# Kernel tuning notes

Measured on AMD Instinct MI355X. Metric: run time of the kernel, lower is better.

## Reference

```python
import jax, jax.numpy as jnp
import numpy as np

B, T, U, V, H, KA, KO = 64, 600, 64, 80, 512, 10, 20


def setup_inputs() -> dict:
    key = jax.random.key(0)
    ks = jax.random.split(key, 12)
    std = 0.075
    p = lambda k, shape: jax.random.normal(k, shape, jnp.float32) * std
    return dict(
        char_seq=jax.random.randint(ks[0], (B, U), 0, V),
        char_mask=jnp.ones((B, U), jnp.float32),
        strokes=jax.random.normal(ks[1], (B, T, 3), jnp.float32),
        strokes_mask=jnp.ones((B, T), jnp.float32),
        lstm0_Wih=p(ks[2], (4 * H, 3 + V)), lstm0_Whh=p(ks[3], (4 * H, H)), lstm0_b=jnp.zeros((4 * H,), jnp.float32),
        win_W=p(ks[4], (3 * KA, H)), win_b=jnp.zeros((3 * KA,), jnp.float32),
        lstm1_Wih=p(ks[5], (4 * H, 3 + V + H)), lstm1_Whh=p(ks[6], (4 * H, H)), lstm1_b=jnp.zeros((4 * H,), jnp.float32),
        lstm2_Wih=p(ks[7], (4 * H, 3 + V + H)), lstm2_Whh=p(ks[8], (4 * H, H)), lstm2_b=jnp.zeros((4 * H,), jnp.float32),
        fc_W=p(ks[9], (6 * KO + 1, 3 * H)), fc_b=jnp.zeros((6 * KO + 1,), jnp.float32),
    )


def _lstm_cell(gates_x, h, c, Whh):
    # gates_x already contains x@Wih.T + b; PyTorch gate order: i, f, g, o
    gates = gates_x + h @ Whh.T
    i, f, g, o = jnp.split(gates, 4, axis=-1)
    c = jax.nn.sigmoid(f) * c + jax.nn.sigmoid(i) * jnp.tanh(g)
    h = jax.nn.sigmoid(o) * jnp.tanh(c)
    return h, c


def _run_lstm(x, Wih, Whh, b):
    # x: [B, T, F]; precompute input projection once (big GEMM), scan only on h.
    gx = jnp.einsum('btf,gf->btg', x, Wih) + b  # [B,T,4H]
    h0 = jnp.zeros((x.shape[0], H), x.dtype)
    c0 = jnp.zeros((x.shape[0], H), x.dtype)

    def step(carry, g_t):
        h, c = carry
        h, c = _lstm_cell(g_t, h, c, Whh)
        return (h, c), h

    _, hs = jax.lax.scan(step, (h0, c0), gx.transpose(1, 0, 2))
    return hs.transpose(1, 0, 2)  # [B,T,H]


def _forward(char_seq, char_mask, strokes,
             lstm0_Wih, lstm0_Whh, lstm0_b, win_W, win_b,
             lstm1_Wih, lstm1_Whh, lstm1_b, lstm2_Wih, lstm2_Whh, lstm2_b,
             fc_W, fc_b):
    char_oh = jax.nn.one_hot(char_seq, V, dtype=jnp.float32) * char_mask[..., None]  # [B,U,V]
    u_grid = jnp.arange(U, dtype=jnp.float32)  # char positions

    h0 = jnp.zeros((B, H), jnp.float32)
    c0 = jnp.zeros((B, H), jnp.float32)
    w0 = jnp.zeros((B, V), jnp.float32)
    k0 = jnp.zeros((B, KA), jnp.float32)

    def step(carry, x_t):
        h, c, w, k = carry
        inp = jnp.concatenate([x_t, w], axis=-1)  # [B, 3+V]
        gates = inp @ lstm0_Wih.T + lstm0_b
        h, c = _lstm_cell(gates, h, c, lstm0_Whh)
        # Gaussian attention window (Graves 2013)
        p = h @ win_W.T + win_b  # [B, 3K]
        alpha, beta, kap_hat = jnp.split(jnp.exp(p), 3, axis=-1)
        k = k + kap_hat  # [B,K]
        phi = jnp.sum(alpha[:, :, None] * jnp.exp(-beta[:, :, None] * (k[:, :, None] - u_grid) ** 2), axis=1)
        phi = phi * char_mask  # [B,U]
        w = jnp.einsum('bu,buv->bv', phi, char_oh)
        return (h, c, w, k), (h, w)

    _, (h_seq, w_seq) = jax.lax.scan(step, (h0, c0, w0, k0), strokes.transpose(1, 0, 2))
    lstm0_out = h_seq.transpose(1, 0, 2)   # [B,T,H]
    attn_out = w_seq.transpose(1, 0, 2)    # [B,T,V]

    lstm1_out = _run_lstm(jnp.concatenate([strokes, attn_out, lstm0_out], -1), lstm1_Wih, lstm1_Whh, lstm1_b)
    lstm2_out = _run_lstm(jnp.concatenate([strokes, attn_out, lstm1_out], -1), lstm2_Wih, lstm2_Whh, lstm2_b)

    final = jnp.einsum('bth,gh->btg', jnp.concatenate([lstm0_out, lstm1_out, lstm2_out], -1), fc_W) + fc_b
    # parse_outputs: split [2K, 2K, K, K, 1]
    myu = final[..., : 2 * KO]
    log_sigma = final[..., 2 * KO: 4 * KO]
    pi = final[..., 4 * KO: 5 * KO]
    rho = final[..., 5 * KO: 6 * KO]
    eos = final[..., 6 * KO:]
    log_pi = jax.nn.log_softmax(pi, axis=-1)
    rho = jnp.tanh(rho)
    eos = jax.nn.sigmoid(-eos)
    myu = myu.reshape(myu.shape[:-1] + (KO, 2))
    log_sigma = log_sigma.reshape(log_sigma.shape[:-1] + (KO, 2))
    return (log_pi, myu, log_sigma, rho, eos)


def reference(char_seq, char_mask, strokes, strokes_mask,
              lstm0_Wih, lstm0_Whh, lstm0_b, win_W, win_b,
              lstm1_Wih, lstm1_Whh, lstm1_b, lstm2_Wih, lstm2_Whh, lstm2_b,
              fc_W, fc_b):
    # strokes_mask is unused by forward() in the original module (only in losses)
    return _forward(char_seq, char_mask, strokes,
                    lstm0_Wih, lstm0_Whh, lstm0_b, win_W, win_b,
                    lstm1_Wih, lstm1_Whh, lstm1_b, lstm2_Wih, lstm2_Whh, lstm2_b,
                    fc_W, fc_b)
```

## Files before the change

kernel.cpp:

```cpp
#include <hip/hip_runtime.h>
#include <math.h>

#define B_ 64
#define T_ 600
#define U_ 64
#define V_ 80
#define H_ 512
#define KA_ 10
#define KO_ 20

#define S0_ 600
#define S12_ 1108

__device__ __forceinline__ float sigmf(float x){ return 1.0f/(1.0f+expf(-x)); }

__device__ __forceinline__ int coh_load_i32(const int* p){
    int v;
    asm volatile("global_load_dword %0, %1, off sc0 sc1\n\ts_waitcnt vmcnt(0)"
                 : "=v"(v) : "v"(p) : "memory");
    return v;
}
__device__ __forceinline__ void coh_store_f32(float* p, float v){
    asm volatile("global_store_dword %0, %1, off sc0 sc1" :: "v"(p), "v"(v) : "memory");
}
__device__ __forceinline__ void coh_store_u32(unsigned* p, unsigned v){
    asm volatile("global_store_dword %0, %1, off sc0 sc1" :: "v"(p), "v"(v) : "memory");
}
__device__ __forceinline__ void spin_ge(int* p, int target){
    while (coh_load_i32(p) < target) __builtin_amdgcn_s_sleep(4);
}
#define BLOCK_WAIT(p, tgt) do { if (threadIdx.x == 0) spin_ge((p), (tgt)); __syncthreads(); } while (0)

__device__ __forceinline__ float blo(unsigned u){ return __uint_as_float(u << 16); }
__device__ __forceinline__ float bhi(unsigned u){ return __uint_as_float(u & 0xffff0000u); }
__device__ __forceinline__ unsigned pack_bf16(float a, float b){
    return ((__float_as_uint(a) + 0x8000u) >> 16) | ((__float_as_uint(b) + 0x8000u) & 0xffff0000u);
}

__global__ __launch_bounds__(64) void k_prep(
    const float* __restrict__ W0ih, const float* __restrict__ W0hh,
    const float* __restrict__ W1ih, const float* __restrict__ W1hh,
    const float* __restrict__ W2ih, const float* __restrict__ W2hh,
    float* __restrict__ wpad)
{
    int r = blockIdx.x;
    int tid = threadIdx.x;
    if (r < 2048){
        float* dst = wpad + (size_t)r*S0_;
        const float* sih = W0ih + (size_t)r*83;
        const float* shh = W0hh + (size_t)r*512;
        if (tid < 3) dst[tid] = sih[tid];
        if (tid == 3) dst[3] = 0.f;
        for (int v=tid; v<V_; v+=64) dst[4+v] = sih[3+v];
        for (int k=tid; k<H_; k+=64) dst[84+k] = shh[k];
    } else {
        int rr = r - 2048;
        int layer = rr >> 11;
        int row = rr & 2047;
        const float* sih = (layer==0 ? W1ih : W2ih) + (size_t)row*595;
        const float* shh = (layer==0 ? W1hh : W2hh) + (size_t)row*512;
        float* dst = wpad + (size_t)2048*S0_ + ((size_t)layer*2048 + row)*S12_;
        if (tid < 3) dst[tid] = sih[tid];
        if (tid == 3) dst[3] = 0.f;
        for (int v=tid; v<V_; v+=64) dst[4+v] = sih[3+v];
        for (int k=tid; k<H_; k+=64) dst[84+k] = sih[83+k];
        for (int k=tid; k<H_; k+=64) dst[596+k] = shh[k];
    }
}

__global__ __launch_bounds__(256, 2) void k_pipe(
    const float* __restrict__ strokes,
    const int*   __restrict__ char_seq,
    const float* __restrict__ char_mask,
    const float* __restrict__ wpad,
    const float* __restrict__ winW, const float* __restrict__ winb,
    const float* __restrict__ b0, const float* __restrict__ b1, const float* __restrict__ b2,
    float* __restrict__ out0, float* __restrict__ out1, float* __restrict__ out2,
    unsigned* __restrict__ attnb, int* __restrict__ sync)
{
    __builtin_amdgcn_fence(__ATOMIC_ACQUIRE, "agent");

    int* c0 = sync;
    int* c1 = sync + 640;
    int* c2 = sync + 1280;
    int* cw = sync + 1920;

    const int bid = blockIdx.x;
    const int tid = threadIdx.x;
    const int b   = tid & 63;
    const int g   = tid >> 6;

    __shared__ float part[4][4][64];
    __shared__ float pp[30][8];
    __shared__ float sa[KA_], sbv[KA_], sk[KA_], skst[KA_];
    __shared__ float sphi[U_];
    __shared__ float satt[V_];
    __shared__ int   sseq[U_];
    __shared__ float smask[U_];

    if (bid >= 384){
        const int wb = bid - 384;
        if (tid < U_){ sseq[tid] = char_seq[wb*U_+tid]; smask[tid] = char_mask[wb*U_+tid]; }
        __syncthreads();
        for (int t=0; t<T_; ++t){
            BLOCK_WAIT(&c0[t], 128);
            if (tid < 240){
                int r = tid >> 3, p8 = tid & 7;
                const float4* hp = (const float4*)(out0 + (size_t)t*32768);
                const float4* wr = (const float4*)(winW + (size_t)r*H_);
                float acc = 0.f;
                int kq0 = p8*16;
                #pragma unroll 4
                for (int i=0; i<16; ++i){
                    float4 xv = hp[(size_t)(kq0+i)*64 + wb];
                    float4 wv = wr[kq0+i];
                    acc += xv.x*wv.x + xv.y*wv.y + xv.z*wv.z + xv.w*wv.w;
                }
                pp[r][p8] = acc;
            }
            __syncthreads();
            if (tid < 30){
                float p = winb[tid];
                #pragma unroll
                for (int i=0; i<8; ++i) p += pp[tid][i];
                float e = expf(p);
                if (tid < KA_) sa[tid] = e;
                else if (tid < 2*KA_) sbv[tid-KA_] = e;
                else {
                    int a2 = tid - 2*KA_;
                    float kn = ((t == 0) ? 0.f : skst[a2]) + e;
                    skst[a2] = kn; sk[a2] = kn;
                }
            }
            __syncthreads();
            if (tid < U_){
                float acc = 0.f;
                #pragma unroll
                for (int a=0; a<KA_; ++a){
                    float d = sk[a] - (float)tid;
                    acc += sa[a]*expf(-sbv[a]*d*d);
                }
                sphi[tid] = acc * smask[tid]*smask[tid];
            }
            __syncthreads();
            if (tid < V_){
                float wv = 0.f;
                for (int u=0; u<U_; ++u) wv += (sseq[u] == tid) ? sphi[u] : 0.f;
                satt[tid] = wv;
            }
            __syncthreads();
            if (tid < 40){
                unsigned pk = pack_bf16(satt[2*tid], satt[2*tid+1]);
                coh_store_u32(attnb + (size_t)t*2560 + (size_t)wb*40 + tid, pk);
            }
            __syncthreads();
            if (tid == 0) atomicAdd(&cw[t], 1);
        }
        return;
    }

    const int l  = bid >> 7;
    const int ub = (bid & 127) * 4;

    const float* wbase; const float* bias_p; const float* xprev; float* outp;
    int* cself; int* cprev; size_t wstride; int roff;
    if (l == 0){ wbase = wpad;                                          wstride = S0_;  bias_p = b0; outp = out0; xprev = nullptr; cself = c0; cprev = nullptr; roff = 84; }
    else if (l == 1){ wbase = wpad + (size_t)2048*S0_;                  wstride = S12_; bias_p = b1; outp = out1; xprev = out0;   cself = c1; cprev = c0;     roff = 596; }
    else { wbase = wpad + (size_t)2048*S0_ + (size_t)2048*S12_;         wstride = S12_; bias_p = b2; outp = out2; xprev = out1;   cself = c2; cprev = c1;     roff = 596; }

    const float* wr = wbase + ((size_t)g*H_ + ub)*wstride;
    const float* wr1 = wr + wstride;
    const float* wr2 = wr + 2*wstride;
    const float* wr3 = wr + 3*wstride;

    const int cu = ub + g;
    const float bgi = bias_p[0*H_+cu];
    const float bgf = bias_p[1*H_+cu];
    const float bgg = bias_p[2*H_+cu];
    const float bgo = bias_p[3*H_+cu];
    float creg = 0.f;

    for (int t=0; t<T_; ++t){
        float a0, a1, a2, a3;
        {
            const float* sr = strokes + ((size_t)b*T_ + t)*3;
            float sx=sr[0], sy=sr[1], sz=sr[2];
            a0 = sx*wr[0]  + sy*wr[1]  + sz*wr[2];
            a1 = sx*wr1[0] + sy*wr1[1] + sz*wr1[2];
            a2 = sx*wr2[0] + sy*wr2[1] + sz*wr2[2];
            a3 = sx*wr3[0] + sy*wr3[1] + sz*wr3[2];
        }
        if (t > 0){
            BLOCK_WAIT(&cself[t-1], 128);
            const float4* hp = (const float4*)(outp + (size_t)(t-1)*32768) + b;
            #pragma unroll 4
            for (int kq=0; kq<128; ++kq){
                float4 xv = hp[kq*64];
                float4 q0 = *(const float4*)(wr  + roff + kq*4);
                float4 q1 = *(const float4*)(wr1 + roff + kq*4);
                float4 q2 = *(const float4*)(wr2 + roff + kq*4);
                float4 q3 = *(const float4*)(wr3 + roff + kq*4);
                a0 += xv.x*q0.x + xv.y*q0.y + xv.z*q0.z + xv.w*q0.w;
                a1 += xv.x*q1.x + xv.y*q1.y + xv.z*q1.z + xv.w*q1.w;
                a2 += xv.x*q2.x + xv.y*q2.y + xv.z*q2.z + xv.w*q2.w;
                a3 += xv.x*q3.x + xv.y*q3.y + xv.z*q3.z + xv.w*q3.w;
            }
        }
        if (l > 0){
            BLOCK_WAIT(&cprev[t], 128);
            const float4* hp = (const float4*)(xprev + (size_t)t*32768) + b;
            #pragma unroll 4
            for (int kq=0; kq<128; ++kq){
                float4 xv = hp[kq*64];
                float4 q0 = *(const float4*)(wr  + 84 + kq*4);
                float4 q1 = *(const float4*)(wr1 + 84 + kq*4);
                float4 q2 = *(const float4*)(wr2 + 84 + kq*4);
                float4 q3 = *(const float4*)(wr3 + 84 + kq*4);
                a0 += xv.x*q0.x + xv.y*q0.y + xv.z*q0.z + xv.w*q0.w;
                a1 += xv.x*q1.x + xv.y*q1.y + xv.z*q1.z + xv.w*q1.w;
                a2 += xv.x*q2.x + xv.y*q2.y + xv.z*q2.z + xv.w*q2.w;
                a3 += xv.x*q3.x + xv.y*q3.y + xv.z*q3.z + xv.w*q3.w;
            }
        }
        {
            int ta = (l == 0) ? (t-1) : t;
            if (ta >= 0){
                BLOCK_WAIT(&cw[ta], 64);
                const uint4* ap = (const uint4*)(attnb + (size_t)ta*2560 + (size_t)b*40);
                #pragma unroll
                for (int j=0; j<10; ++j){
                    uint4 q = ap[j];
                    float x0 = blo(q.x), x1 = bhi(q.x), x2 = blo(q.y), x3 = bhi(q.y);
                    float x4 = blo(q.z), x5 = bhi(q.z), x6 = blo(q.w), x7 = bhi(q.w);
                    float4 qa, qb;
                    qa = *(const float4*)(wr  + 4 + 8*j); qb = *(const float4*)(wr  + 8 + 8*j);
                    a0 += x0*qa.x + x1*qa.y + x2*qa.z + x3*qa.w + x4*qb.x + x5*qb.y + x6*qb.z + x7*qb.w;
                    qa = *(const float4*)(wr1 + 4 + 8*j); qb = *(const float4*)(wr1 + 8 + 8*j);
                    a1 += x0*qa.x + x1*qa.y + x2*qa.z + x3*qa.w + x4*qb.x + x5*qb.y + x6*qb.z + x7*qb.w;
                    qa = *(const float4*)(wr2 + 4 + 8*j); qb = *(const float4*)(wr2 + 8 + 8*j);
                    a2 += x0*qa.x + x1*qa.y + x2*qa.z + x3*qa.w + x4*qb.x + x5*qb.y + x6*qb.z + x7*qb.w;
                    qa = *(const float4*)(wr3 + 4 + 8*j); qb = *(const float4*)(wr3 + 8 + 8*j);
                    a3 += x0*qa.x + x1*qa.y + x2*qa.z + x3*qa.w + x4*qb.x + x5*qb.y + x6*qb.z + x7*qb.w;
                }
            }
        }
        part[g][0][b] = a0;
        part[g][1][b] = a1;
        part[g][2][b] = a2;
        part[g][3][b] = a3;
        __syncthreads();
        {
            float gi  = part[0][g][b] + bgi;
            float gf  = part[1][g][b] + bgf;
            float gg_ = part[2][g][b] + bgg;
            float go  = part[3][g][b] + bgo;
            float cold = (t == 0) ? 0.f : creg;
            float cnew = sigmf(gf)*cold + sigmf(gi)*tanhf(gg_);
            creg = cnew;
            float h = sigmf(go)*tanhf(cnew);
            coh_store_f32(outp + (size_t)t*32768 + (size_t)(cu>>2)*256 + b*4 + (cu&3), h);
        }
        __syncthreads();
        if (tid == 0) atomicAdd(&cself[t], 1);
    }
}

__global__ __launch_bounds__(256) void k_fc(
    const float* __restrict__ out0, const float* __restrict__ out1, const float* __restrict__ out2,
    const float* __restrict__ fcW, const float* __restrict__ fcb, float* __restrict__ out)
{
    int t = blockIdx.x; int tid = threadIdx.x;
    int b = tid & 63; int gq = tid >> 6;
    __shared__ float smraw[128*65];

    float acc[31];
    #pragma unroll
    for (int i=0; i<31; ++i) acc[i] = 0.f;

    const float* outs[3] = {out0, out1, out2};
    for (int seg=0; seg<3; ++seg){
        const float* o = outs[seg] + (size_t)t*32768;
        for (int kc=0; kc<H_; kc+=128){
            __syncthreads();
            #pragma unroll
            for (int r=0; r<8; ++r){
                int idx = tid + 256*r;
                int kql = idx >> 6;
                int bb  = idx & 63;
                float4 v = *(const float4*)(o + (size_t)((kc>>2) + kql)*256 + bb*4);
                smraw[(4*kql+0)*65+bb] = v.x;
                smraw[(4*kql+1)*65+bb] = v.y;
                smraw[(4*kql+2)*65+bb] = v.z;
                smraw[(4*kql+3)*65+bb] = v.w;
            }
            __syncthreads();
            for (int kk=0; kk<128; kk+=4){
                float a0 = smraw[(kk+0)*65+b];
                float a1 = smraw[(kk+1)*65+b];
                float a2 = smraw[(kk+2)*65+b];
                float a3 = smraw[(kk+3)*65+b];
                int K = seg*H_ + kc + kk;
                #pragma unroll
                for (int i=0; i<30; ++i){
                    float4 w = *(const float4*)(fcW + (size_t)(gq+4*i)*1536 + K);
                    acc[i] += a0*w.x + a1*w.y + a2*w.z + a3*w.w;
                }
                if (gq == 0){
                    float4 w = *(const float4*)(fcW + (size_t)120*1536 + K);
                    acc[30] += a0*w.x + a1*w.y + a2*w.z + a3*w.w;
                }
            }
        }
    }
    __syncthreads();
    #pragma unroll
    for (int i=0; i<30; ++i) smraw[(gq+4*i)*64 + b] = acc[i] + fcb[gq+4*i];
    if (gq == 0) smraw[120*64 + b] = acc[30] + fcb[120];
    __syncthreads();

    if (tid < 64){
        size_t bt = (size_t)b*T_ + t;
        float* myu = out + 768000;
        #pragma unroll
        for (int q=0; q<10; ++q){
            float4 v;
            v.x = smraw[(4*q+0)*64+b]; v.y = smraw[(4*q+1)*64+b];
            v.z = smraw[(4*q+2)*64+b]; v.w = smraw[(4*q+3)*64+b];
            *(float4*)(myu + bt*40 + 4*q) = v;
        }
        float* lsg = out + 2304000;
        #pragma unroll
        for (int q=0; q<10; ++q){
            float4 v;
            v.x = smraw[(40+4*q+0)*64+b]; v.y = smraw[(40+4*q+1)*64+b];
            v.z = smraw[(40+4*q+2)*64+b]; v.w = smraw[(40+4*q+3)*64+b];
            *(float4*)(lsg + bt*40 + 4*q) = v;
        }
        float pi[KO_];
        float m = -1e30f;
        #pragma unroll
        for (int ko=0; ko<KO_; ++ko){ pi[ko] = smraw[(80+ko)*64+b]; m = fmaxf(m, pi[ko]); }
        float s = 0.f;
        #pragma unroll
        for (int ko=0; ko<KO_; ++ko) s += expf(pi[ko]-m);
        float lse = m + logf(s);
        #pragma unroll
        for (int q=0; q<5; ++q){
            float4 v;
            v.x = pi[4*q+0]-lse; v.y = pi[4*q+1]-lse; v.z = pi[4*q+2]-lse; v.w = pi[4*q+3]-lse;
            *(float4*)(out + bt*20 + 4*q) = v;
        }
        float* rho = out + 3840000;
        #pragma unroll
        for (int q=0; q<5; ++q){
            float4 v;
            v.x = tanhf(smraw[(100+4*q+0)*64+b]); v.y = tanhf(smraw[(100+4*q+1)*64+b]);
            v.z = tanhf(smraw[(100+4*q+2)*64+b]); v.w = tanhf(smraw[(100+4*q+3)*64+b]);
            *(float4*)(rho + bt*20 + 4*q) = v;
        }
        out[4608000 + bt] = 1.f/(1.f + expf(smraw[120*64+b]));
    }
}

extern "C" void kernel_launch(void* const* d_in, const int* in_sizes, int n_in,
                              void* d_out, int out_size, void* d_ws, size_t ws_size,
                              hipStream_t stream)
{
    const int*   char_seq  = (const int*)  d_in[0];
    const float* char_mask = (const float*)d_in[1];
    const float* strokes   = (const float*)d_in[2];
    const float* W0ih = (const float*)d_in[4];
    const float* W0hh = (const float*)d_in[5];
    const float* b0   = (const float*)d_in[6];
    const float* winW = (const float*)d_in[7];
    const float* winb = (const float*)d_in[8];
    const float* W1ih = (const float*)d_in[9];
    const float* W1hh = (const float*)d_in[10];
    const float* b1   = (const float*)d_in[11];
    const float* W2ih = (const float*)d_in[12];
    const float* W2hh = (const float*)d_in[13];
    const float* b2   = (const float*)d_in[14];
    const float* fcW  = (const float*)d_in[15];
    const float* fcb  = (const float*)d_in[16];

    float* ws   = (float*)d_ws;
    float*    out0  = ws;
    float*    out1  = out0 + 19660800;
    float*    out2  = out1 + 19660800;
    unsigned* attnb = (unsigned*)(out2 + 19660800);
    float*    wpad  = (float*)(attnb + 1536000);
    int*      sync  = (int*)(wpad + 5767168);

    hipMemsetAsync(sync, 0, 2560*sizeof(int), stream);

    hipLaunchKernelGGL(k_prep, dim3(6144), dim3(64), 0, stream,
        W0ih, W0hh, W1ih, W1hh, W2ih, W2hh, wpad);

    hipLaunchKernelGGL(k_pipe, dim3(448), dim3(256), 0, stream,
        strokes, char_seq, char_mask, wpad, winW, winb, b0, b1, b2,
        out0, out1, out2, attnb, sync);

    hipLaunchKernelGGL(k_fc, dim3(600), dim3(256), 0, stream,
        out0, out1, out2, fcW, fcb, (float*)d_out);
}
```

Measured before the change: 53.08 ms.

## Restructure LSTM pipeline: bf16 hidden states, 8 units per block, fewer blocks

Hidden-state outputs of all three LSTM layers are now stored as packed bf16 instead of fp32, which halves inter-block traffic and the fc input reads. Each pipeline block now has 512 threads, and each thread computes all four gates for one unit over the full K range. This removes the shared-memory cross-gate reduction and halves the number of LSTM blocks (64 per layer). The window blocks stage the hidden state in shared memory and use 480 threads for the projection. Layers 1 and 2 wait on all dependencies at once, and the spin sleep is shorter. The change risks reduced precision and a longer serial dot product per thread.

```diff
diff --git a/kernel.cpp b/kernel.cpp
--- a/kernel.cpp
+++ b/kernel.cpp
@@ -11,6 +11,10 @@
 
 #define S0_ 600
 #define S12_ 1108
+#define NLB_ 64
+#define NWB_ 64
+
+typedef unsigned u32x4 __attribute__((ext_vector_type(4)));
 
 __device__ __forceinline__ float sigmf(float x){ return 1.0f/(1.0f+expf(-x)); }
 
@@ -20,14 +24,14 @@
                  : "=v"(v) : "v"(p) : "memory");
     return v;
 }
-__device__ __forceinline__ void coh_store_f32(float* p, float v){
-    asm volatile("global_store_dword %0, %1, off sc0 sc1" :: "v"(p), "v"(v) : "memory");
-}
 __device__ __forceinline__ void coh_store_u32(unsigned* p, unsigned v){
     asm volatile("global_store_dword %0, %1, off sc0 sc1" :: "v"(p), "v"(v) : "memory");
 }
+__device__ __forceinline__ void coh_store_u128(unsigned* p, u32x4 v){
+    asm volatile("global_store_dwordx4 %0, %1, off sc0 sc1" :: "v"(p), "v"(v) : "memory");
+}
 __device__ __forceinline__ void spin_ge(int* p, int target){
-    while (coh_load_i32(p) < target) __builtin_amdgcn_s_sleep(4);
+    while (coh_load_i32(p) < target) __builtin_amdgcn_s_sleep(1);
 }
 #define BLOCK_WAIT(p, tgt) do { if (threadIdx.x == 0) spin_ge((p), (tgt)); __syncthreads(); } while (0)
 
@@ -68,14 +72,20 @@
     }
 }
 
-__global__ __launch_bounds__(256, 2) void k_pipe(
+#define FMA8(W, OFF) do { \
+    float4 qa = *(const float4*)((W) + (OFF)); \
+    float4 qb = *(const float4*)((W) + (OFF) + 4); \
+    A0 += x0*qa.x + x1*qa.y + x2*qa.z + x3*qa.w + x4*qb.x + x5*qb.y + x6*qb.z + x7*qb.w; \
+} while (0)
+
+__global__ __launch_bounds__(512, 2) void k_pipe(
     const float* __restrict__ strokes,
     const int*   __restrict__ char_seq,
     const float* __restrict__ char_mask,
     const float* __restrict__ wpad,
     const float* __restrict__ winW, const float* __restrict__ winb,
     const float* __restrict__ b0, const float* __restrict__ b1, const float* __restrict__ b2,
-    float* __restrict__ out0, float* __restrict__ out1, float* __restrict__ out2,
+    unsigned* __restrict__ out0b, unsigned* __restrict__ out1b, unsigned* __restrict__ out2b,
     unsigned* __restrict__ attnb, int* __restrict__ sync)
 {
     __builtin_amdgcn_fence(__ATOMIC_ACQUIRE, "agent");
@@ -88,42 +98,45 @@
     const int bid = blockIdx.x;
     const int tid = threadIdx.x;
     const int b   = tid & 63;
-    const int g   = tid >> 6;
-
-    __shared__ float part[4][4][64];
-    __shared__ float pp[30][8];
+    const int r   = tid >> 6;
+
+    __shared__ float sh[8][64];
+    __shared__ float shh[512];
+    __shared__ float pp[30][16];
     __shared__ float sa[KA_], sbv[KA_], sk[KA_], skst[KA_];
     __shared__ float sphi[U_];
     __shared__ float satt[V_];
     __shared__ int   sseq[U_];
     __shared__ float smask[U_];
 
-    if (bid >= 384){
-        const int wb = bid - 384;
+    if (bid >= 192){
+        const int wb = bid - 192;
         if (tid < U_){ sseq[tid] = char_seq[wb*U_+tid]; smask[tid] = char_mask[wb*U_+tid]; }
         __syncthreads();
         for (int t=0; t<T_; ++t){
-            BLOCK_WAIT(&c0[t], 128);
-            if (tid < 240){
-                int r = tid >> 3, p8 = tid & 7;
-                const float4* hp = (const float4*)(out0 + (size_t)t*32768);
-                const float4* wr = (const float4*)(winW + (size_t)r*H_);
+            BLOCK_WAIT(&c0[t], NLB_);
+            if (tid < 64){
+                uint4 q = ((const uint4*)out0b)[((size_t)t*64 + tid)*64 + wb];
+                shh[8*tid+0]=blo(q.x); shh[8*tid+1]=bhi(q.x);
+                shh[8*tid+2]=blo(q.y); shh[8*tid+3]=bhi(q.y);
+                shh[8*tid+4]=blo(q.z); shh[8*tid+5]=bhi(q.z);
+                shh[8*tid+6]=blo(q.w); shh[8*tid+7]=bhi(q.w);
+            }
+            __syncthreads();
+            if (tid < 480){
+                int rr = tid >> 4, p = tid & 15;
+                const float* wrow = winW + (size_t)rr*H_;
                 float acc = 0.f;
-                int kq0 = p8*16;
-                #pragma unroll 4
-                for (int i=0; i<16; ++i){
-                    float4 xv = hp[(size_t)(kq0+i)*64 + wb];
-                    float4 wv = wr[kq0+i];
-                    acc += xv.x*wv.x + xv.y*wv.y + xv.z*wv.z + xv.w*wv.w;
-                }
-                pp[r][p8] = acc;
+                #pragma unroll 8
+                for (int i=0; i<32; ++i) acc += shh[p+16*i]*wrow[p+16*i];
+                pp[rr][p] = acc;
             }
             __syncthreads();
             if (tid < 30){
-                float p = winb[tid];
+                float pv = winb[tid];
                 #pragma unroll
-                for (int i=0; i<8; ++i) p += pp[tid][i];
-                float e = expf(p);
+                for (int i=0; i<16; ++i) pv += pp[tid][i];
+                float e = expf(pv);
                 if (tid < KA_) sa[tid] = e;
                 else if (tid < 2*KA_) sbv[tid-KA_] = e;
                 else {
@@ -150,8 +163,9 @@
             }
             __syncthreads();
             if (tid < 40){
-                unsigned pk = pack_bf16(satt[2*tid], satt[2*tid+1]);
-                coh_store_u32(attnb + (size_t)t*2560 + (size_t)wb*40 + tid, pk);
+                coh_store_u32(attnb + (size_t)t*2560 + (size_t)wb*40 + tid,
+                              pack_bf16(satt[2*tid], satt[2*tid+1]));
+                asm volatile("s_waitcnt vmcnt(0)" ::: "memory");
             }
             __syncthreads();
             if (tid == 0) atomicAdd(&cw[t], 1);
@@ -159,25 +173,25 @@
         return;
     }
 
-    const int l  = bid >> 7;
-    const int ub = (bid & 127) * 4;
-
-    const float* wbase; const float* bias_p; const float* xprev; float* outp;
-    int* cself; int* cprev; size_t wstride; int roff;
-    if (l == 0){ wbase = wpad;                                          wstride = S0_;  bias_p = b0; outp = out0; xprev = nullptr; cself = c0; cprev = nullptr; roff = 84; }
-    else if (l == 1){ wbase = wpad + (size_t)2048*S0_;                  wstride = S12_; bias_p = b1; outp = out1; xprev = out0;   cself = c1; cprev = c0;     roff = 596; }
-    else { wbase = wpad + (size_t)2048*S0_ + (size_t)2048*S12_;         wstride = S12_; bias_p = b2; outp = out2; xprev = out1;   cself = c2; cprev = c1;     roff = 596; }
-
-    const float* wr = wbase + ((size_t)g*H_ + ub)*wstride;
-    const float* wr1 = wr + wstride;
-    const float* wr2 = wr + 2*wstride;
-    const float* wr3 = wr + 3*wstride;
-
-    const int cu = ub + g;
-    const float bgi = bias_p[0*H_+cu];
-    const float bgf = bias_p[1*H_+cu];
-    const float bgg = bias_p[2*H_+cu];
-    const float bgo = bias_p[3*H_+cu];
+    const int l  = bid >> 6;
+    const int ub = (bid & 63) * 8;
+    const int cu = ub + r;
+
+    const float* wbase; const float* bias_p; size_t wst;
+    unsigned* hbo; const unsigned* hbp; int* cself; int* cprev;
+    if (l == 0){ wbase = wpad;                                  wst = S0_;  bias_p = b0; hbo = out0b; hbp = nullptr; cself = c0; cprev = nullptr; }
+    else if (l == 1){ wbase = wpad + (size_t)2048*S0_;          wst = S12_; bias_p = b1; hbo = out1b; hbp = out0b;  cself = c1; cprev = c0; }
+    else { wbase = wpad + (size_t)2048*S0_ + (size_t)2048*S12_; wst = S12_; bias_p = b2; hbo = out2b; hbp = out1b;  cself = c2; cprev = c1; }
+
+    const float* w0 = wbase + (size_t)(0*H_+cu)*wst;
+    const float* w1 = wbase + (size_t)(1*H_+cu)*wst;
+    const float* w2 = wbase + (size_t)(2*H_+cu)*wst;
+    const float* w3 = wbase + (size_t)(3*H_+cu)*wst;
+
+    const float bq0 = bias_p[0*H_+cu];
+    const float bq1 = bias_p[1*H_+cu];
+    const float bq2 = bias_p[2*H_+cu];
+    const float bq3 = bias_p[3*H_+cu];
     float creg = 0.f;
 
     for (int t=0; t<T_; ++t){
@@ -185,80 +199,120 @@
         {
             const float* sr = strokes + ((size_t)b*T_ + t)*3;
             float sx=sr[0], sy=sr[1], sz=sr[2];
-            a0 = sx*wr[0]  + sy*wr[1]  + sz*wr[2];
-            a1 = sx*wr1[0] + sy*wr1[1] + sz*wr1[2];
-            a2 = sx*wr2[0] + sy*wr2[1] + sz*wr2[2];
-            a3 = sx*wr3[0] + sy*wr3[1] + sz*wr3[2];
-        }
-        if (t > 0){
-            BLOCK_WAIT(&cself[t-1], 128);
-            const float4* hp = (const float4*)(outp + (size_t)(t-1)*32768) + b;
-            #pragma unroll 4
-            for (int kq=0; kq<128; ++kq){
-                float4 xv = hp[kq*64];
-                float4 q0 = *(const float4*)(wr  + roff + kq*4);
-                float4 q1 = *(const float4*)(wr1 + roff + kq*4);
-                float4 q2 = *(const float4*)(wr2 + roff + kq*4);
-                float4 q3 = *(const float4*)(wr3 + roff + kq*4);
-                a0 += xv.x*q0.x + xv.y*q0.y + xv.z*q0.z + xv.w*q0.w;
-                a1 += xv.x*q1.x + xv.y*q1.y + xv.z*q1.z + xv.w*q1.w;
-                a2 += xv.x*q2.x + xv.y*q2.y + xv.z*q2.z + xv.w*q2.w;
-                a3 += xv.x*q3.x + xv.y*q3.y + xv.z*q3.z + xv.w*q3.w;
-            }
-        }
-        if (l > 0){
-            BLOCK_WAIT(&cprev[t], 128);
-            const float4* hp = (const float4*)(xprev + (size_t)t*32768) + b;
-            #pragma unroll 4
-            for (int kq=0; kq<128; ++kq){
-                float4 xv = hp[kq*64];
-                float4 q0 = *(const float4*)(wr  + 84 + kq*4);
-                float4 q1 = *(const float4*)(wr1 + 84 + kq*4);
-                float4 q2 = *(const float4*)(wr2 + 84 + kq*4);
-                float4 q3 = *(const float4*)(wr3 + 84 + kq*4);
-                a0 += xv.x*q0.x + xv.y*q0.y + xv.z*q0.z + xv.w*q0.w;
-                a1 += xv.x*q1.x + xv.y*q1.y + xv.z*q1.z + xv.w*q1.w;
-                a2 += xv.x*q2.x + xv.y*q2.y + xv.z*q2.z + xv.w*q2.w;
-                a3 += xv.x*q3.x + xv.y*q3.y + xv.z*q3.z + xv.w*q3.w;
-            }
-        }
-        {
-            int ta = (l == 0) ? (t-1) : t;
-            if (ta >= 0){
-                BLOCK_WAIT(&cw[ta], 64);
-                const uint4* ap = (const uint4*)(attnb + (size_t)ta*2560 + (size_t)b*40);
+            a0 = sx*w0[0] + sy*w0[1] + sz*w0[2];
+            a1 = sx*w1[0] + sy*w1[1] + sz*w1[2];
+            a2 = sx*w2[0] + sy*w2[1] + sz*w2[2];
+            a3 = sx*w3[0] + sy*w3[1] + sz*w3[2];
+        }
+
+        if (l == 0){
+            if (t > 0){
+                BLOCK_WAIT(&c0[t-1], NLB_);
+                const uint4* hp = (const uint4*)out0b + (size_t)(t-1)*4096 + b;
+                #pragma unroll 4
+                for (int kp=0; kp<64; ++kp){
+                    uint4 q = hp[(size_t)kp*64];
+                    float x0=blo(q.x),x1=bhi(q.x),x2=blo(q.y),x3=bhi(q.y);
+                    float x4=blo(q.z),x5=bhi(q.z),x6=blo(q.w),x7=bhi(q.w);
+                    int o = 84 + 8*kp;
+                    { float A0=a0; FMA8(w0,o); a0=A0; }
+                    { float A0=a1; FMA8(w1,o); a1=A0; }
+                    { float A0=a2; FMA8(w2,o); a2=A0; }
+                    { float A0=a3; FMA8(w3,o); a3=A0; }
+                }
+                BLOCK_WAIT(&cw[t-1], NWB_);
+                const uint4* ap = (const uint4*)(attnb + (size_t)(t-1)*2560 + (size_t)b*40);
                 #pragma unroll
                 for (int j=0; j<10; ++j){
                     uint4 q = ap[j];
-                    float x0 = blo(q.x), x1 = bhi(q.x), x2 = blo(q.y), x3 = bhi(q.y);
-                    float x4 = blo(q.z), x5 = bhi(q.z), x6 = blo(q.w), x7 = bhi(q.w);
-                    float4 qa, qb;
-                    qa = *(const float4*)(wr  + 4 + 8*j); qb = *(const float4*)(wr  + 8 + 8*j);
-                    a0 += x0*qa.x + x1*qa.y + x2*qa.z + x3*qa.w + x4*qb.x + x5*qb.y + x6*qb.z + x7*qb.w;
-                    qa = *(const float4*)(wr1 + 4 + 8*j); qb = *(const float4*)(wr1 + 8 + 8*j);
-                    a1 += x0*qa.x + x1*qa.y + x2*qa.z + x3*qa.w + x4*qb.x + x5*qb.y + x6*qb.z + x7*qb.w;
-                    qa = *(const float4*)(wr2 + 4 + 8*j); qb = *(const float4*)(wr2 + 8 + 8*j);
-                    a2 += x0*qa.x + x1*qa.y + x2*qa.z + x3*qa.w + x4*qb.x + x5*qb.y + x6*qb.z + x7*qb.w;
-                    qa = *(const float4*)(wr3 + 4 + 8*j); qb = *(const float4*)(wr3 + 8 + 8*j);
-                    a3 += x0*qa.x + x1*qa.y + x2*qa.z + x3*qa.w + x4*qb.x + x5*qb.y + x6*qb.z + x7*qb.w;
-                }
-            }
-        }
-        part[g][0][b] = a0;
-        part[g][1][b] = a1;
-        part[g][2][b] = a2;
-        part[g][3][b] = a3;
-        __syncthreads();
+                    float x0=blo(q.x),x1=bhi(q.x),x2=blo(q.y),x3=bhi(q.y);
+                    float x4=blo(q.z),x5=bhi(q.z),x6=blo(q.w),x7=bhi(q.w);
+                    int o = 4 + 8*j;
+                    { float A0=a0; FMA8(w0,o); a0=A0; }
+                    { float A0=a1; FMA8(w1,o); a1=A0; }
+                    { float A0=a2; FMA8(w2,o); a2=A0; }
+                    { float A0=a3; FMA8(w3,o); a3=A0; }
+                }
+            }
+        } else {
+            if (tid == 0){
+                if (t > 0) spin_ge(&cself[t-1], NLB_);
+                spin_ge(&cprev[t], NLB_);
+                spin_ge(&cw[t], NWB_);
+            }
+            __syncthreads();
+            const uint4* hc = (const uint4*)hbp + (size_t)t*4096 + b;
+            if (t > 0){
+                const uint4* ho = (const uint4*)hbo + (size_t)(t-1)*4096 + b;
+                #pragma unroll 2
+                for (int kp=0; kp<64; ++kp){
+                    uint4 qo = ho[(size_t)kp*64];
+                    uint4 qc = hc[(size_t)kp*64];
+                    {
+                        float x0=blo(qo.x),x1=bhi(qo.x),x2=blo(qo.y),x3=bhi(qo.y);
+                        float x4=blo(qo.z),x5=bhi(qo.z),x6=blo(qo.w),x7=bhi(qo.w);
+                        int o = 596 + 8*kp;
+                        { float A0=a0; FMA8(w0,o); a0=A0; }
+                        { float A0=a1; FMA8(w1,o); a1=A0; }
+                        { float A0=a2; FMA8(w2,o); a2=A0; }
+                        { float A0=a3; FMA8(w3,o); a3=A0; }
+                    }
+                    {
+                        float x0=blo(qc.x),x1=bhi(qc.x),x2=blo(qc.y),x3=bhi(qc.y);
+                        float x4=blo(qc.z),x5=bhi(qc.z),x6=blo(qc.w),x7=bhi(qc.w);
+                        int o = 84 + 8*kp;
+                        { float A0=a0; FMA8(w0,o); a0=A0; }
+                        { float A0=a1; FMA8(w1,o); a1=A0; }
+                        { float A0=a2; FMA8(w2,o); a2=A0; }
+                        { float A0=a3; FMA8(w3,o); a3=A0; }
+                    }
+                }
+            } else {
+                #pragma unroll 4
+                for (int kp=0; kp<64; ++kp){
+                    uint4 qc = hc[(size_t)kp*64];
+                    float x0=blo(qc.x),x1=bhi(qc.x),x2=blo(qc.y),x3=bhi(qc.y);
+                    float x4=blo(qc.z),x5=bhi(qc.z),x6=blo(qc.w),x7=bhi(qc.w);
+                    int o = 84 + 8*kp;
+                    { float A0=a0; FMA8(w0,o); a0=A0; }
+                    { float A0=a1; FMA8(w1,o); a1=A0; }
+                    { float A0=a2; FMA8(w2,o); a2=A0; }
+                    { float A0=a3; FMA8(w3,o); a3=A0; }
+                }
+            }
+            const uint4* ap = (const uint4*)(attnb + (size_t)t*2560 + (size_t)b*40);
+            #pragma unroll
+            for (int j=0; j<10; ++j){
+                uint4 q = ap[j];
+                float x0=blo(q.x),x1=bhi(q.x),x2=blo(q.y),x3=bhi(q.y);
+                float x4=blo(q.z),x5=bhi(q.z),x6=blo(q.w),x7=bhi(q.w);
+                int o = 4 + 8*j;
+                { float A0=a0; FMA8(w0,o); a0=A0; }
+                { float A0=a1; FMA8(w1,o); a1=A0; }
+                { float A0=a2; FMA8(w2,o); a2=A0; }
+                { float A0=a3; FMA8(w3,o); a3=A0; }
+            }
+        }
+
         {
-            float gi  = part[0][g][b] + bgi;
-            float gf  = part[1][g][b] + bgf;
-            float gg_ = part[2][g][b] + bgg;
-            float go  = part[3][g][b] + bgo;
+            float gi  = a0 + bq0;
+            float gf  = a1 + bq1;
+            float gg_ = a2 + bq2;
+            float go  = a3 + bq3;
             float cold = (t == 0) ? 0.f : creg;
             float cnew = sigmf(gf)*cold + sigmf(gi)*tanhf(gg_);
             creg = cnew;
-            float h = sigmf(go)*tanhf(cnew);
-            coh_store_f32(outp + (size_t)t*32768 + (size_t)(cu>>2)*256 + b*4 + (cu&3), h);
+            sh[r][b] = sigmf(go)*tanhf(cnew);
+        }
+        __syncthreads();
+        if (tid < 64){
+            u32x4 v;
+            v.x = pack_bf16(sh[0][tid], sh[1][tid]);
+            v.y = pack_bf16(sh[2][tid], sh[3][tid]);
+            v.z = pack_bf16(sh[4][tid], sh[5][tid]);
+            v.w = pack_bf16(sh[6][tid], sh[7][tid]);
+            coh_store_u128(hbo + (size_t)t*16384 + (size_t)(ub>>3)*256 + tid*4, v);
+            asm volatile("s_waitcnt vmcnt(0)" ::: "memory");
         }
         __syncthreads();
         if (tid == 0) atomicAdd(&cself[t], 1);
@@ -266,7 +320,7 @@
 }
 
 __global__ __launch_bounds__(256) void k_fc(
-    const float* __restrict__ out0, const float* __restrict__ out1, const float* __restrict__ out2,
+    const unsigned* __restrict__ out0b, const unsigned* __restrict__ out1b, const unsigned* __restrict__ out2b,
     const float* __restrict__ fcW, const float* __restrict__ fcb, float* __restrict__ out)
 {
     int t = blockIdx.x; int tid = threadIdx.x;
@@ -277,21 +331,23 @@
     #pragma unroll
     for (int i=0; i<31; ++i) acc[i] = 0.f;
 
-    const float* outs[3] = {out0, out1, out2};
+    const unsigned* hbs[3] = {out0b, out1b, out2b};
     for (int seg=0; seg<3; ++seg){
-        const float* o = outs[seg] + (size_t)t*32768;
+        const uint4* o = (const uint4*)hbs[seg];
         for (int kc=0; kc<H_; kc+=128){
+            int kp0 = kc >> 3;
             __syncthreads();
             #pragma unroll
-            for (int r=0; r<8; ++r){
-                int idx = tid + 256*r;
-                int kql = idx >> 6;
+            for (int rr=0; rr<4; ++rr){
+                int idx = tid + 256*rr;
+                int kq  = idx >> 6;
                 int bb  = idx & 63;
-                float4 v = *(const float4*)(o + (size_t)((kc>>2) + kql)*256 + bb*4);
-                smraw[(4*kql+0)*65+bb] = v.x;
-                smraw[(4*kql+1)*65+bb] = v.y;
-                smraw[(4*kql+2)*65+bb] = v.z;
-                smraw[(4*kql+3)*65+bb] = v.w;
+                uint4 v = o[((size_t)t*64 + kp0 + kq)*64 + bb];
+                int kb = kq*8;
+                smraw[(kb+0)*65+bb]=blo(v.x); smraw[(kb+1)*65+bb]=bhi(v.x);
+                smraw[(kb+2)*65+bb]=blo(v.y); smraw[(kb+3)*65+bb]=bhi(v.y);
+                smraw[(kb+4)*65+bb]=blo(v.z); smraw[(kb+5)*65+bb]=bhi(v.z);
+                smraw[(kb+6)*65+bb]=blo(v.w); smraw[(kb+7)*65+bb]=bhi(v.w);
             }
             __syncthreads();
             for (int kk=0; kk<128; kk+=4){
@@ -383,23 +439,22 @@
     const float* fcW  = (const float*)d_in[15];
     const float* fcb  = (const float*)d_in[16];
 
-    float* ws   = (float*)d_ws;
-    float*    out0  = ws;
-    float*    out1  = out0 + 19660800;
-    float*    out2  = out1 + 19660800;
-    unsigned* attnb = (unsigned*)(out2 + 19660800);
+    unsigned* out0b = (unsigned*)d_ws;
+    unsigned* out1b = out0b + 9830400;
+    unsigned* out2b = out1b + 9830400;
+    unsigned* attnb = out2b + 9830400;
     float*    wpad  = (float*)(attnb + 1536000);
     int*      sync  = (int*)(wpad + 5767168);
 
-    hipMemsetAsync(sync, 0, 2560*sizeof(int), stream);
+    (void)hipMemsetAsync(sync, 0, 2560*sizeof(int), stream);
 
     hipLaunchKernelGGL(k_prep, dim3(6144), dim3(64), 0, stream,
         W0ih, W0hh, W1ih, W1hh, W2ih, W2hh, wpad);
 
-    hipLaunchKernelGGL(k_pipe, dim3(448), dim3(256), 0, stream,
+    hipLaunchKernelGGL(k_pipe, dim3(256), dim3(512), 0, stream,
         strokes, char_seq, char_mask, wpad, winW, winb, b0, b1, b2,
-        out0, out1, out2, attnb, sync);
+        out0b, out1b, out2b, attnb, sync);
 
     hipLaunchKernelGGL(k_fc, dim3(600), dim3(256), 0, stream,
-        out0, out1, out2, fcW, fcb, (float*)d_out);
-}
+        out0b, out1b, out2b, fcW, fcb, (float*)d_out);
+}
```

Result: slower. 54.57 ms (+2.8%).
